# Performance work log

Hardware: AMD Instinct MI355X
Metric: run time of the kernel (lower is better)

The kernel has to match this reference:

```python
import jax, jax.numpy as jnp
import numpy as np

B, S, D, H = 2, 2048, 1024, 16
HD = D // H  # head dim = 64


def setup_inputs() -> dict:
    key = jax.random.key(0)
    ks = jax.random.split(key, 8)
    s = 0.02
    return {
        "Q": jax.random.normal(ks[0], (B, S, D), jnp.float32),
        "K": jax.random.normal(ks[1], (B, S, D), jnp.float32),
        "V": jax.random.normal(ks[2], (B, S, D), jnp.float32),
        "mask": jax.random.randint(ks[3], (1, 1, S, S), 0, 2, jnp.int32),
        "Wq": jax.random.normal(ks[4], (D, D), jnp.float32) * s,
        "bq": jnp.zeros((D,), jnp.float32),
        "Wk": jax.random.normal(ks[5], (D, D), jnp.float32) * s,
        "bk": jnp.zeros((D,), jnp.float32),
        "Wv": jax.random.normal(ks[6], (D, D), jnp.float32) * s,
        "bv": jnp.zeros((D,), jnp.float32),
        "Wo": jax.random.normal(ks[7], (D, D), jnp.float32) * s,
        "bo": jnp.zeros((D,), jnp.float32),
    }


def reference(Q, K, V, mask, Wq, bq, Wk, bk, Wv, bv, Wo, bo):
    b = Q.shape[0]
    # QKV projections, split into heads: [B,S,D] -> [B,H,S,HD]
    q = (Q @ Wq + bq).reshape(b, -1, H, HD).transpose(0, 2, 1, 3)
    k = (K @ Wk + bk).reshape(b, -1, H, HD).transpose(0, 2, 1, 3)
    v = (V @ Wv + bv).reshape(b, -1, H, HD).transpose(0, 2, 1, 3)
    # scaled dot-product attention with full [B,H,S,S] scores (as in source)
    scale = jnp.sqrt(jnp.asarray(HD, q.dtype))
    scores = jnp.einsum("bhqd,bhkd->bhqk", q, k) / scale
    scores = jnp.where(mask == 0, -jnp.inf, scores)
    attn = jax.nn.softmax(scores, axis=-1)
    ctx = jnp.einsum("bhqk,bhkd->bhqd", attn, v)
    # merge heads and output projection
    concat = ctx.transpose(0, 2, 1, 3).reshape(b, -1, H * HD)
    return concat @ Wo + bo
```

## Files before the change

### kernel.cpp

```cpp
#include <hip/hip_runtime.h>


using s8v = __attribute__((ext_vector_type(8))) short;
using f4v = __attribute__((ext_vector_type(4))) float;
typedef unsigned long long u64;

__device__ __forceinline__ unsigned short f2bf(float f) {
  union { float f; unsigned int u; } v; v.f = f;
  return (unsigned short)((v.u + 0x7fffu + ((v.u >> 16) & 1u)) >> 16);
}

__global__ void f2b3_kernel(const float* __restrict__ A, const float* __restrict__ B,
                            const float* __restrict__ C, unsigned short* __restrict__ oA,
                            unsigned short* __restrict__ oB, unsigned short* __restrict__ oC) {
  int z = blockIdx.x >> 12;
  int idx = (blockIdx.x & 4095) * 256 + threadIdx.x;
  const float* in = (z == 0) ? A : (z == 1) ? B : C;
  unsigned short* out = (z == 0) ? oA : (z == 1) ? oB : oC;
  float4 v = ((const float4*)in)[idx];
  ushort4 o;
  o.x = f2bf(v.x); o.y = f2bf(v.y); o.z = f2bf(v.z); o.w = f2bf(v.w);
  ((ushort4*)out)[idx] = o;
}

__global__ void packmask_kernel(const int* __restrict__ mask, u64* __restrict__ bm) {
  int gw = (int)((blockIdx.x * 256 + threadIdx.x) >> 6);
  int lane = threadIdx.x & 63;
  int mv = mask[(size_t)gw * 64 + lane];
  u64 bal = __ballot(mv != 0);
  if (lane == 0) bm[gw] = bal;
}

__global__ void wtrans4_kernel(const float* __restrict__ W0, const float* __restrict__ W1,
                               const float* __restrict__ W2, const float* __restrict__ W3,
                               unsigned short* __restrict__ T0, unsigned short* __restrict__ T1,
                               unsigned short* __restrict__ T2, unsigned short* __restrict__ T3) {
  __shared__ unsigned short t[64][72];
  int z = blockIdx.z;
  const float* W = (z == 0) ? W0 : (z == 1) ? W1 : (z == 2) ? W2 : W3;
  unsigned short* Wt = (z == 0) ? T0 : (z == 1) ? T1 : (z == 2) ? T2 : T3;
  int k0 = blockIdx.x * 64, n0 = blockIdx.y * 64;
  int tid = threadIdx.x;
  for (int p = 0; p < 4; ++p) {
    int idx = p * 256 + tid;
    int row = idx >> 4;
    int c4  = idx & 15;
    float4 v = *(const float4*)&W[(size_t)(k0 + row) * 1024 + n0 + c4 * 4];
    t[row][c4 * 4 + 0] = f2bf(v.x);
    t[row][c4 * 4 + 1] = f2bf(v.y);
    t[row][c4 * 4 + 2] = f2bf(v.z);
    t[row][c4 * 4 + 3] = f2bf(v.w);
  }
  __syncthreads();
  for (int p = 0; p < 2; ++p) {
    int idx = p * 256 + tid;
    int j  = idx >> 3;
    int c8 = idx & 7;
    unsigned short tmp[8];
    for (int i = 0; i < 8; ++i) tmp[i] = t[c8 * 8 + i][j];
    uint4 o;
    o.x = tmp[0] | ((unsigned)tmp[1] << 16);
    o.y = tmp[2] | ((unsigned)tmp[3] << 16);
    o.z = tmp[4] | ((unsigned)tmp[5] << 16);
    o.w = tmp[6] | ((unsigned)tmp[7] << 16);
    *(uint4*)&Wt[(size_t)(n0 + j) * 1024 + k0 + c8 * 8] = o;
  }
}

__global__ __launch_bounds__(256) void proj3_kernel(
    const unsigned short* __restrict__ A0, const unsigned short* __restrict__ A1,
    const unsigned short* __restrict__ A2,
    const unsigned short* __restrict__ W0, const unsigned short* __restrict__ W1,
    const unsigned short* __restrict__ W2,
    const float* __restrict__ b0, const float* __restrict__ b1, const float* __restrict__ b2,
    unsigned short* __restrict__ oq, unsigned short* __restrict__ ok,
    unsigned short* __restrict__ ovt) {
  const int z = blockIdx.z;
  const unsigned short* A  = (z == 0) ? A0 : (z == 1) ? A1 : A2;
  const unsigned short* Wt = (z == 0) ? W0 : (z == 1) ? W1 : W2;
  const float* bias        = (z == 0) ? b0 : (z == 1) ? b1 : b2;

  __shared__ __align__(16) unsigned short As[128][40];
  __shared__ __align__(16) unsigned short Bs[128][40];

  const int tid = threadIdx.x;
  const int lane = tid & 63, w = tid >> 6, ln = lane & 15, quad = lane >> 4;
  const int wm = (w & 1) * 64, wn = (w >> 1) * 64;
  const int m0 = blockIdx.x * 128, n0 = blockIdx.y * 128;

  const int r0 = tid >> 2, c40 = tid & 3;
  const int r1 = (tid + 256) >> 2, c41 = tid & 3;

  uint4 ar0 = *(const uint4*)&A[(size_t)(m0 + r0) * 1024 + c40 * 8];
  uint4 ar1 = *(const uint4*)&A[(size_t)(m0 + r1) * 1024 + c41 * 8];
  uint4 br0 = *(const uint4*)&Wt[(size_t)(n0 + r0) * 1024 + c40 * 8];
  uint4 br1 = *(const uint4*)&Wt[(size_t)(n0 + r1) * 1024 + c41 * 8];

  f4v zero = {0.f, 0.f, 0.f, 0.f};
  f4v acc[4][4];
  for (int mi = 0; mi < 4; ++mi)
    for (int ni = 0; ni < 4; ++ni) acc[mi][ni] = zero;

  for (int kt = 0; kt < 1024; kt += 32) {
    *(uint4*)&As[r0][c40 * 8] = ar0;
    *(uint4*)&As[r1][c41 * 8] = ar1;
    *(uint4*)&Bs[r0][c40 * 8] = br0;
    *(uint4*)&Bs[r1][c41 * 8] = br1;
    if (kt + 32 < 1024) {
      ar0 = *(const uint4*)&A[(size_t)(m0 + r0) * 1024 + kt + 32 + c40 * 8];
      ar1 = *(const uint4*)&A[(size_t)(m0 + r1) * 1024 + kt + 32 + c41 * 8];
      br0 = *(const uint4*)&Wt[(size_t)(n0 + r0) * 1024 + kt + 32 + c40 * 8];
      br1 = *(const uint4*)&Wt[(size_t)(n0 + r1) * 1024 + kt + 32 + c41 * 8];
    }
    __syncthreads();
    s8v a[4], b[4];
    for (int mi = 0; mi < 4; ++mi) a[mi] = *(const s8v*)&As[wm + mi * 16 + ln][quad * 8];
    for (int ni = 0; ni < 4; ++ni) b[ni] = *(const s8v*)&Bs[wn + ni * 16 + ln][quad * 8];
    for (int mi = 0; mi < 4; ++mi)
      for (int ni = 0; ni < 4; ++ni)
        acc[mi][ni] = __builtin_amdgcn_mfma_f32_16x16x32_bf16(a[mi], b[ni], acc[mi][ni], 0, 0, 0);
    __syncthreads();
  }

  const float qscale = (z == 0) ? 0.18033688f : 1.0f;
  if (z < 2) {
    unsigned short* outp = (z == 0) ? oq : ok;
    for (int mi = 0; mi < 4; ++mi) {
      int rb = m0 + wm + mi * 16 + quad * 4;
      int b_ = rb >> 11;
      for (int ni = 0; ni < 4; ++ni) {
        int col = n0 + wn + ni * 16 + ln;
        float bvv = bias[col];
        int h = col >> 6, hd = col & 63;
        size_t ob = (size_t)(b_ * 16 + h) * 2048;
        for (int r = 0; r < 4; ++r) {
          int s = (rb + r) & 2047;
          outp[(ob + s) * 64 + hd] = f2bf((acc[mi][ni][r] + bvv) * qscale);
        }
      }
    }
  } else {
    for (int mi = 0; mi < 4; ++mi) {
      int rb = m0 + wm + mi * 16 + quad * 4;
      int b_ = rb >> 11, s = rb & 2047;
      for (int ni = 0; ni < 4; ++ni) {
        int col = n0 + wn + ni * 16 + ln;
        float bvv = bias[col];
        int h = col >> 6, hd = col & 63;
        ushort4 o;
        o.x = f2bf(acc[mi][ni][0] + bvv);
        o.y = f2bf(acc[mi][ni][1] + bvv);
        o.z = f2bf(acc[mi][ni][2] + bvv);
        o.w = f2bf(acc[mi][ni][3] + bvv);
        *(ushort4*)&ovt[((size_t)(b_ * 16 + h) * 64 + hd) * 2048 + s] = o;
      }
    }
  }
}

__global__ __launch_bounds__(256) void flash_kernel(
    const unsigned short* __restrict__ q, const unsigned short* __restrict__ k,
    const unsigned short* __restrict__ vt, const u64* __restrict__ bm,
    unsigned short* __restrict__ ctx) {
  __shared__ __align__(16) unsigned short qp_s[128][72];
  __shared__ __align__(16) unsigned short k_s[64][72];
  __shared__ __align__(16) unsigned short v_s[64][72];

  const int tid = threadIdx.x;
  const int lane = tid & 63, w = tid >> 6, ln = lane & 15, quad = lane >> 4;
  const int q0 = blockIdx.x * 128;
  const int bh = blockIdx.y;
  const unsigned short* qg  = q  + ((size_t)bh * 2048 + q0) * 64;
  const unsigned short* kgb = k  + (size_t)bh * 2048 * 64;
  const unsigned short* vgb = vt + (size_t)bh * 64 * 2048;

  for (int p = 0; p < 4; ++p) {
    int c = p * 256 + tid;
    int row = c >> 3, c8 = c & 7;
    *(uint4*)&qp_s[row][c8 * 8] = *(const uint4*)&qg[(size_t)row * 64 + c8 * 8];
  }
  __syncthreads();
  s8v aq[2][2];
  for (int s = 0; s < 2; ++s)
    for (int h = 0; h < 2; ++h)
      aq[s][h] = *(const s8v*)&qp_s[s * 64 + w * 16 + ln][h * 32 + quad * 8];

  const int srow0 = tid >> 3, sc8 = tid & 7;
  const int srow1 = 32 + srow0;

  const u64* bmr0 = bm + (size_t)(q0 + w * 16 + ln) * 32;
  const u64* bmr1 = bmr0 + 64 * 32;

  uint4 kr0 = *(const uint4*)&kgb[(size_t)srow0 * 64 + sc8 * 8];
  uint4 kr1 = *(const uint4*)&kgb[(size_t)srow1 * 64 + sc8 * 8];
  uint4 vr0 = *(const uint4*)&vgb[(size_t)srow0 * 2048 + sc8 * 8];
  uint4 vr1 = *(const uint4*)&vgb[(size_t)srow1 * 2048 + sc8 * 8];
  u64 mwc[2], mwn[2];
  mwc[0] = bmr0[0];
  mwc[1] = bmr1[0];

  f4v zero = {0.f, 0.f, 0.f, 0.f};
  float lsum[2] = {0.f, 0.f};
  f4v o_acc[2][4];
  for (int s = 0; s < 2; ++s)
    for (int ni = 0; ni < 4; ++ni) o_acc[s][ni] = zero;

  for (int kt = 0; kt < 2048; kt += 64) {
    *(uint4*)&k_s[srow0][sc8 * 8] = kr0;
    *(uint4*)&k_s[srow1][sc8 * 8] = kr1;
    *(uint4*)&v_s[srow0][sc8 * 8] = vr0;
    *(uint4*)&v_s[srow1][sc8 * 8] = vr1;
    if (kt + 64 < 2048) {
      int ktn = kt + 64;
      kr0 = *(const uint4*)&kgb[(size_t)(ktn + srow0) * 64 + sc8 * 8];
      kr1 = *(const uint4*)&kgb[(size_t)(ktn + srow1) * 64 + sc8 * 8];
      vr0 = *(const uint4*)&vgb[(size_t)srow0 * 2048 + ktn + sc8 * 8];
      vr1 = *(const uint4*)&vgb[(size_t)srow1 * 2048 + ktn + sc8 * 8];
      int ktcn = ktn >> 6;
      mwn[0] = bmr0[ktcn];
      mwn[1] = bmr1[ktcn];
    }
    __syncthreads();

    f4v sc[2][4];
    for (int ni = 0; ni < 4; ++ni) {
      s8v ak0 = *(const s8v*)&k_s[ni * 16 + ln][quad * 8];
      s8v ak1 = *(const s8v*)&k_s[ni * 16 + ln][32 + quad * 8];
      for (int s = 0; s < 2; ++s) {
        f4v t = zero;
        t = __builtin_amdgcn_mfma_f32_16x16x32_bf16(ak0, aq[s][0], t, 0, 0, 0);
        t = __builtin_amdgcn_mfma_f32_16x16x32_bf16(ak1, aq[s][1], t, 0, 0, 0);
        sc[s][ni] = t;
      }
    }

    for (int s = 0; s < 2; ++s) {
      u64 m = mwc[s] >> (quad * 4);
      unsigned mlo = (unsigned)m, mhi = (unsigned)(m >> 32);
      float lacc = 0.f;
      for (int ni = 0; ni < 4; ++ni) {
        unsigned msel = ((ni < 2) ? mlo : mhi) >> ((ni & 1) * 16);
        u64 pk = 0;
        for (int r = 0; r < 4; ++r) {
          float e = __builtin_amdgcn_exp2f(sc[s][ni][r]) * (float)((msel >> r) & 1u);
          unsigned u = __float_as_uint(e);
          lacc += __uint_as_float(u & 0xffff0000u);
          pk |= (u64)(u >> 16) << (16 * r);
        }
        *(u64*)&qp_s[s * 64 + w * 16 + ln][ni * 16 + quad * 4] = pk;
      }
      lsum[s] += lacc;
      mwc[s] = mwn[s];
    }

    s8v ap[2][2];
    for (int s = 0; s < 2; ++s)
      for (int h = 0; h < 2; ++h)
        ap[s][h] = *(const s8v*)&qp_s[s * 64 + w * 16 + ln][h * 32 + quad * 8];
    for (int ni = 0; ni < 4; ++ni) {
      s8v bv0 = *(const s8v*)&v_s[ni * 16 + ln][quad * 8];
      s8v bv1 = *(const s8v*)&v_s[ni * 16 + ln][32 + quad * 8];
      for (int s = 0; s < 2; ++s) {
        o_acc[s][ni] = __builtin_amdgcn_mfma_f32_16x16x32_bf16(ap[s][0], bv0, o_acc[s][ni], 0, 0, 0);
        o_acc[s][ni] = __builtin_amdgcn_mfma_f32_16x16x32_bf16(ap[s][1], bv1, o_acc[s][ni], 0, 0, 0);
      }
    }
    __syncthreads();
  }

  int b_ = bh >> 4, h = bh & 15;
  for (int s = 0; s < 2; ++s) {
    float l = lsum[s];
    l += __shfl_xor(l, 16);
    l += __shfl_xor(l, 32);
    for (int r = 0; r < 4; ++r) {
      float lr = __shfl(l, quad * 4 + r);
      float inv = 1.f / lr;
      int srow = q0 + s * 64 + w * 16 + quad * 4 + r;
      size_t base = ((size_t)b_ * 2048 + srow) * 1024 + h * 64;
      for (int ni = 0; ni < 4; ++ni)
        ctx[base + ni * 16 + ln] = f2bf(o_acc[s][ni][r] * inv);
    }
  }
}

__global__ __launch_bounds__(256) void gemm_out_kernel(
    const unsigned short* __restrict__ A, const unsigned short* __restrict__ Wt,
    const float* __restrict__ bias, float* __restrict__ out) {
  __shared__ __align__(16) unsigned short As[128][40];
  __shared__ __align__(16) unsigned short Bs[128][40];

  const int tid = threadIdx.x;
  const int lane = tid & 63, w = tid >> 6, ln = lane & 15, quad = lane >> 4;
  const int wm = (w & 1) * 64, wn = (w >> 1) * 64;
  const int m0 = blockIdx.x * 128, n0 = blockIdx.y * 128;

  const int r0 = tid >> 2, c40 = tid & 3;
  const int r1 = (tid + 256) >> 2, c41 = tid & 3;

  uint4 ar0 = *(const uint4*)&A[(size_t)(m0 + r0) * 1024 + c40 * 8];
  uint4 ar1 = *(const uint4*)&A[(size_t)(m0 + r1) * 1024 + c41 * 8];
  uint4 br0 = *(const uint4*)&Wt[(size_t)(n0 + r0) * 1024 + c40 * 8];
  uint4 br1 = *(const uint4*)&Wt[(size_t)(n0 + r1) * 1024 + c41 * 8];

  f4v zero = {0.f, 0.f, 0.f, 0.f};
  f4v acc[4][4];
  for (int mi = 0; mi < 4; ++mi)
    for (int ni = 0; ni < 4; ++ni) acc[mi][ni] = zero;

  for (int kt = 0; kt < 1024; kt += 32) {
    *(uint4*)&As[r0][c40 * 8] = ar0;
    *(uint4*)&As[r1][c41 * 8] = ar1;
    *(uint4*)&Bs[r0][c40 * 8] = br0;
    *(uint4*)&Bs[r1][c41 * 8] = br1;
    if (kt + 32 < 1024) {
      ar0 = *(const uint4*)&A[(size_t)(m0 + r0) * 1024 + kt + 32 + c40 * 8];
      ar1 = *(const uint4*)&A[(size_t)(m0 + r1) * 1024 + kt + 32 + c41 * 8];
      br0 = *(const uint4*)&Wt[(size_t)(n0 + r0) * 1024 + kt + 32 + c40 * 8];
      br1 = *(const uint4*)&Wt[(size_t)(n0 + r1) * 1024 + kt + 32 + c41 * 8];
    }
    __syncthreads();
    s8v a[4], b[4];
    for (int mi = 0; mi < 4; ++mi) a[mi] = *(const s8v*)&As[wm + mi * 16 + ln][quad * 8];
    for (int ni = 0; ni < 4; ++ni) b[ni] = *(const s8v*)&Bs[wn + ni * 16 + ln][quad * 8];
    for (int mi = 0; mi < 4; ++mi)
      for (int ni = 0; ni < 4; ++ni)
        acc[mi][ni] = __builtin_amdgcn_mfma_f32_16x16x32_bf16(a[mi], b[ni], acc[mi][ni], 0, 0, 0);
    __syncthreads();
  }

  for (int mi = 0; mi < 4; ++mi) {
    int rb = m0 + wm + mi * 16 + quad * 4;
    for (int ni = 0; ni < 4; ++ni) {
      int col = n0 + wn + ni * 16 + ln;
      float bvv = bias[col];
      for (int r = 0; r < 4; ++r)
        out[(size_t)(rb + r) * 1024 + col] = acc[mi][ni][r] + bvv;
    }
  }
}

extern "C" void kernel_launch(void* const* d_in, const int* in_sizes, int n_in,
                              void* d_out, int out_size, void* d_ws, size_t ws_size,
                              hipStream_t stream) {
  const float* Q  = (const float*)d_in[0];
  const float* K  = (const float*)d_in[1];
  const float* V  = (const float*)d_in[2];
  const int* mask = (const int*)d_in[3];
  const float* Wq = (const float*)d_in[4];
  const float* bq = (const float*)d_in[5];
  const float* Wk = (const float*)d_in[6];
  const float* bk = (const float*)d_in[7];
  const float* Wv = (const float*)d_in[8];
  const float* bv = (const float*)d_in[9];
  const float* Wo = (const float*)d_in[10];
  const float* bo = (const float*)d_in[11];
  float* out = (float*)d_out;

  char* ws = (char*)d_ws;
  const size_t MB = 1u << 20;
  unsigned short* qb  = (unsigned short*)(ws + 0 * MB);
  unsigned short* kb  = (unsigned short*)(ws + 8 * MB);
  unsigned short* vb  = (unsigned short*)(ws + 16 * MB);
  unsigned short* wqt = (unsigned short*)(ws + 24 * MB);
  unsigned short* wkt = (unsigned short*)(ws + 26 * MB);
  unsigned short* wvt = (unsigned short*)(ws + 28 * MB);
  unsigned short* wot = (unsigned short*)(ws + 30 * MB);
  unsigned short* qh  = (unsigned short*)(ws + 32 * MB);
  unsigned short* kh  = (unsigned short*)(ws + 40 * MB);
  unsigned short* vth = (unsigned short*)(ws + 48 * MB);
  unsigned short* ctx = (unsigned short*)(ws + 56 * MB);
  u64* bm = (u64*)(ws + 0 * MB);

  f2b3_kernel<<<12288, 256, 0, stream>>>(Q, K, V, qb, kb, vb);
  wtrans4_kernel<<<dim3(16, 16, 4), 256, 0, stream>>>(Wq, Wk, Wv, Wo, wqt, wkt, wvt, wot);
  proj3_kernel<<<dim3(32, 8, 3), 256, 0, stream>>>(qb, kb, vb, wqt, wkt, wvt,
                                                   bq, bk, bv, qh, kh, vth);
  packmask_kernel<<<16384, 256, 0, stream>>>(mask, bm);
  flash_kernel<<<dim3(16, 32), 256, 0, stream>>>(qh, kh, vth, bm, ctx);
  gemm_out_kernel<<<dim3(32, 8), 256, 0, stream>>>(ctx, wot, bo, out);
}
```

Measured before the change: 270.8 us.

## Use direct global-to-LDS loads with swizzle, MFMA row sums, transposed V store

Both GEMM kernels now stage tiles with global_load_lds into an XOR-swizzled, unpadded LDS layout instead of register-staged loads, which drops the register prefetch and its software pipelining. The V projection swaps MFMA operands so the transposed V output is written with coalesced scalar stores along the sequence. The flash kernel computes softmax row sums with an extra MFMA against a ones matrix instead of scalar accumulation plus shuffles. It also packs exponentials to bf16 with perm instructions. This trades overlap of global loads with compute for lower VGPR use and fewer instructions, and adds MFMA work for the row sums.

```diff
diff --git a/kernel.cpp b/kernel.cpp
--- a/kernel.cpp
+++ b/kernel.cpp
@@ -8,6 +8,12 @@
 __device__ __forceinline__ unsigned short f2bf(float f) {
   union { float f; unsigned int u; } v; v.f = f;
   return (unsigned short)((v.u + 0x7fffu + ((v.u >> 16) & 1u)) >> 16);
+}
+
+__device__ __forceinline__ void gll16(const void* g, void* l) {
+  __builtin_amdgcn_global_load_lds(
+      (const __attribute__((address_space(1))) unsigned int*)g,
+      (__attribute__((address_space(3))) unsigned int*)l, 16, 0, 0);
 }
 
 __global__ void f2b3_kernel(const float* __restrict__ A, const float* __restrict__ B,
@@ -43,8 +49,7 @@
   int tid = threadIdx.x;
   for (int p = 0; p < 4; ++p) {
     int idx = p * 256 + tid;
-    int row = idx >> 4;
-    int c4  = idx & 15;
+    int row = idx >> 4, c4 = idx & 15;
     float4 v = *(const float4*)&W[(size_t)(k0 + row) * 1024 + n0 + c4 * 4];
     t[row][c4 * 4 + 0] = f2bf(v.x);
     t[row][c4 * 4 + 1] = f2bf(v.y);
@@ -54,8 +59,7 @@
   __syncthreads();
   for (int p = 0; p < 2; ++p) {
     int idx = p * 256 + tid;
-    int j  = idx >> 3;
-    int c8 = idx & 7;
+    int j = idx >> 3, c8 = idx & 7;
     unsigned short tmp[8];
     for (int i = 0; i < 8; ++i) tmp[i] = t[c8 * 8 + i][j];
     uint4 o;
@@ -80,21 +84,17 @@
   const unsigned short* Wt = (z == 0) ? W0 : (z == 1) ? W1 : W2;
   const float* bias        = (z == 0) ? b0 : (z == 1) ? b1 : b2;
 
-  __shared__ __align__(16) unsigned short As[128][40];
-  __shared__ __align__(16) unsigned short Bs[128][40];
+  __shared__ __align__(16) unsigned short As[128 * 32];
+  __shared__ __align__(16) unsigned short Bs[128 * 32];
 
   const int tid = threadIdx.x;
   const int lane = tid & 63, w = tid >> 6, ln = lane & 15, quad = lane >> 4;
   const int wm = (w & 1) * 64, wn = (w >> 1) * 64;
   const int m0 = blockIdx.x * 128, n0 = blockIdx.y * 128;
 
-  const int r0 = tid >> 2, c40 = tid & 3;
-  const int r1 = (tid + 256) >> 2, c41 = tid & 3;
-
-  uint4 ar0 = *(const uint4*)&A[(size_t)(m0 + r0) * 1024 + c40 * 8];
-  uint4 ar1 = *(const uint4*)&A[(size_t)(m0 + r1) * 1024 + c41 * 8];
-  uint4 br0 = *(const uint4*)&Wt[(size_t)(n0 + r0) * 1024 + c40 * 8];
-  uint4 br1 = *(const uint4*)&Wt[(size_t)(n0 + r1) * 1024 + c41 * 8];
+  const int srow = w * 32 + (lane >> 2);
+  const int schunk = (lane & 3) ^ ((lane >> 2) & 3);
+  const int cfrag = (quad ^ (ln & 3)) * 8;
 
   f4v zero = {0.f, 0.f, 0.f, 0.f};
   f4v acc[4][4];
@@ -102,28 +102,28 @@
     for (int ni = 0; ni < 4; ++ni) acc[mi][ni] = zero;
 
   for (int kt = 0; kt < 1024; kt += 32) {
-    *(uint4*)&As[r0][c40 * 8] = ar0;
-    *(uint4*)&As[r1][c41 * 8] = ar1;
-    *(uint4*)&Bs[r0][c40 * 8] = br0;
-    *(uint4*)&Bs[r1][c41 * 8] = br1;
-    if (kt + 32 < 1024) {
-      ar0 = *(const uint4*)&A[(size_t)(m0 + r0) * 1024 + kt + 32 + c40 * 8];
-      ar1 = *(const uint4*)&A[(size_t)(m0 + r1) * 1024 + kt + 32 + c41 * 8];
-      br0 = *(const uint4*)&Wt[(size_t)(n0 + r0) * 1024 + kt + 32 + c40 * 8];
-      br1 = *(const uint4*)&Wt[(size_t)(n0 + r1) * 1024 + kt + 32 + c41 * 8];
-    }
+    __syncthreads();
+    gll16(&A[(size_t)(m0 + srow) * 1024 + kt + schunk * 8],       &As[(w * 32) * 32]);
+    gll16(&A[(size_t)(m0 + srow + 16) * 1024 + kt + schunk * 8],  &As[(w * 32 + 16) * 32]);
+    gll16(&Wt[(size_t)(n0 + srow) * 1024 + kt + schunk * 8],      &Bs[(w * 32) * 32]);
+    gll16(&Wt[(size_t)(n0 + srow + 16) * 1024 + kt + schunk * 8], &Bs[(w * 32 + 16) * 32]);
     __syncthreads();
     s8v a[4], b[4];
-    for (int mi = 0; mi < 4; ++mi) a[mi] = *(const s8v*)&As[wm + mi * 16 + ln][quad * 8];
-    for (int ni = 0; ni < 4; ++ni) b[ni] = *(const s8v*)&Bs[wn + ni * 16 + ln][quad * 8];
-    for (int mi = 0; mi < 4; ++mi)
-      for (int ni = 0; ni < 4; ++ni)
-        acc[mi][ni] = __builtin_amdgcn_mfma_f32_16x16x32_bf16(a[mi], b[ni], acc[mi][ni], 0, 0, 0);
-    __syncthreads();
-  }
-
-  const float qscale = (z == 0) ? 0.18033688f : 1.0f;
+    for (int mi = 0; mi < 4; ++mi) a[mi] = *(const s8v*)&As[(wm + mi * 16 + ln) * 32 + cfrag];
+    for (int ni = 0; ni < 4; ++ni) b[ni] = *(const s8v*)&Bs[(wn + ni * 16 + ln) * 32 + cfrag];
+    if (z < 2) {
+      for (int mi = 0; mi < 4; ++mi)
+        for (int ni = 0; ni < 4; ++ni)
+          acc[mi][ni] = __builtin_amdgcn_mfma_f32_16x16x32_bf16(a[mi], b[ni], acc[mi][ni], 0, 0, 0);
+    } else {
+      for (int mi = 0; mi < 4; ++mi)
+        for (int ni = 0; ni < 4; ++ni)
+          acc[mi][ni] = __builtin_amdgcn_mfma_f32_16x16x32_bf16(b[ni], a[mi], acc[mi][ni], 0, 0, 0);
+    }
+  }
+
   if (z < 2) {
+    const float qscale = (z == 0) ? 0.18033688f : 1.0f;
     unsigned short* outp = (z == 0) ? oq : ok;
     for (int mi = 0; mi < 4; ++mi) {
       int rb = m0 + wm + mi * 16 + quad * 4;
@@ -140,19 +140,16 @@
       }
     }
   } else {
-    for (int mi = 0; mi < 4; ++mi) {
-      int rb = m0 + wm + mi * 16 + quad * 4;
-      int b_ = rb >> 11, s = rb & 2047;
-      for (int ni = 0; ni < 4; ++ni) {
-        int col = n0 + wn + ni * 16 + ln;
-        float bvv = bias[col];
-        int h = col >> 6, hd = col & 63;
-        ushort4 o;
-        o.x = f2bf(acc[mi][ni][0] + bvv);
-        o.y = f2bf(acc[mi][ni][1] + bvv);
-        o.z = f2bf(acc[mi][ni][2] + bvv);
-        o.w = f2bf(acc[mi][ni][3] + bvv);
-        *(ushort4*)&ovt[((size_t)(b_ * 16 + h) * 64 + hd) * 2048 + s] = o;
+    for (int ni = 0; ni < 4; ++ni) {
+      for (int r = 0; r < 4; ++r) {
+        int colw = n0 + wn + ni * 16 + quad * 4 + r;
+        int h = colw >> 6, hd = colw & 63;
+        float bvv = bias[colw];
+        for (int mi = 0; mi < 4; ++mi) {
+          int sg = m0 + wm + mi * 16 + ln;
+          int b_ = sg >> 11, ss = sg & 2047;
+          ovt[((size_t)(b_ * 16 + h) * 64 + hd) * 2048 + ss] = f2bf(acc[mi][ni][r] + bvv);
+        }
       }
     }
   }
@@ -164,7 +161,7 @@
     unsigned short* __restrict__ ctx) {
   __shared__ __align__(16) unsigned short qp_s[128][72];
   __shared__ __align__(16) unsigned short k_s[64][72];
-  __shared__ __align__(16) unsigned short v_s[64][72];
+  __shared__ __align__(16) unsigned short v_s[80][72];
 
   const int tid = threadIdx.x;
   const int lane = tid & 63, w = tid >> 6, ln = lane & 15, quad = lane >> 4;
@@ -174,16 +171,25 @@
   const unsigned short* kgb = k  + (size_t)bh * 2048 * 64;
   const unsigned short* vgb = vt + (size_t)bh * 64 * 2048;
 
+  for (int j = 0; j < 5; ++j) {
+    int idx = j * 256 + tid;
+    if (idx < 16 * 72) ((unsigned short*)v_s[64])[idx] = 0;
+  }
   for (int p = 0; p < 4; ++p) {
     int c = p * 256 + tid;
     int row = c >> 3, c8 = c & 7;
     *(uint4*)&qp_s[row][c8 * 8] = *(const uint4*)&qg[(size_t)row * 64 + c8 * 8];
   }
   __syncthreads();
+  if (tid < 64) v_s[64][tid] = 0x3F80;
+  __syncthreads();
+
   s8v aq[2][2];
   for (int s = 0; s < 2; ++s)
     for (int h = 0; h < 2; ++h)
       aq[s][h] = *(const s8v*)&qp_s[s * 64 + w * 16 + ln][h * 32 + quad * 8];
+  s8v bones0 = *(const s8v*)&v_s[64 + ln][quad * 8];
+  s8v bones1 = *(const s8v*)&v_s[64 + ln][32 + quad * 8];
 
   const int srow0 = tid >> 3, sc8 = tid & 7;
   const int srow1 = 32 + srow0;
@@ -200,10 +206,12 @@
   mwc[1] = bmr1[0];
 
   f4v zero = {0.f, 0.f, 0.f, 0.f};
-  float lsum[2] = {0.f, 0.f};
+  f4v l_acc[2];
   f4v o_acc[2][4];
-  for (int s = 0; s < 2; ++s)
+  for (int s = 0; s < 2; ++s) {
+    l_acc[s] = zero;
     for (int ni = 0; ni < 4; ++ni) o_acc[s][ni] = zero;
+  }
 
   for (int kt = 0; kt < 2048; kt += 64) {
     *(uint4*)&k_s[srow0][sc8 * 8] = kr0;
@@ -237,19 +245,16 @@
     for (int s = 0; s < 2; ++s) {
       u64 m = mwc[s] >> (quad * 4);
       unsigned mlo = (unsigned)m, mhi = (unsigned)(m >> 32);
-      float lacc = 0.f;
       for (int ni = 0; ni < 4; ++ni) {
         unsigned msel = ((ni < 2) ? mlo : mhi) >> ((ni & 1) * 16);
-        u64 pk = 0;
-        for (int r = 0; r < 4; ++r) {
-          float e = __builtin_amdgcn_exp2f(sc[s][ni][r]) * (float)((msel >> r) & 1u);
-          unsigned u = __float_as_uint(e);
-          lacc += __uint_as_float(u & 0xffff0000u);
-          pk |= (u64)(u >> 16) << (16 * r);
-        }
-        *(u64*)&qp_s[s * 64 + w * 16 + ln][ni * 16 + quad * 4] = pk;
-      }
-      lsum[s] += lacc;
+        unsigned u0 = __float_as_uint(__builtin_amdgcn_exp2f(sc[s][ni][0]) * (float)(msel & 1u));
+        unsigned u1 = __float_as_uint(__builtin_amdgcn_exp2f(sc[s][ni][1]) * (float)((msel >> 1) & 1u));
+        unsigned u2 = __float_as_uint(__builtin_amdgcn_exp2f(sc[s][ni][2]) * (float)((msel >> 2) & 1u));
+        unsigned u3 = __float_as_uint(__builtin_amdgcn_exp2f(sc[s][ni][3]) * (float)((msel >> 3) & 1u));
+        unsigned plo = __builtin_amdgcn_perm(u1, u0, 0x07060302);
+        unsigned phi = __builtin_amdgcn_perm(u3, u2, 0x07060302);
+        *(u64*)&qp_s[s * 64 + w * 16 + ln][ni * 16 + quad * 4] = plo | ((u64)phi << 32);
+      }
       mwc[s] = mwn[s];
     }
 
@@ -265,16 +270,17 @@
         o_acc[s][ni] = __builtin_amdgcn_mfma_f32_16x16x32_bf16(ap[s][1], bv1, o_acc[s][ni], 0, 0, 0);
       }
     }
+    for (int s = 0; s < 2; ++s) {
+      l_acc[s] = __builtin_amdgcn_mfma_f32_16x16x32_bf16(ap[s][0], bones0, l_acc[s], 0, 0, 0);
+      l_acc[s] = __builtin_amdgcn_mfma_f32_16x16x32_bf16(ap[s][1], bones1, l_acc[s], 0, 0, 0);
+    }
     __syncthreads();
   }
 
   int b_ = bh >> 4, h = bh & 15;
   for (int s = 0; s < 2; ++s) {
-    float l = lsum[s];
-    l += __shfl_xor(l, 16);
-    l += __shfl_xor(l, 32);
     for (int r = 0; r < 4; ++r) {
-      float lr = __shfl(l, quad * 4 + r);
+      float lr = __shfl(l_acc[s][r], quad * 16);
       float inv = 1.f / lr;
       int srow = q0 + s * 64 + w * 16 + quad * 4 + r;
       size_t base = ((size_t)b_ * 2048 + srow) * 1024 + h * 64;
@@ -287,21 +293,17 @@
 __global__ __launch_bounds__(256) void gemm_out_kernel(
     const unsigned short* __restrict__ A, const unsigned short* __restrict__ Wt,
     const float* __restrict__ bias, float* __restrict__ out) {
-  __shared__ __align__(16) unsigned short As[128][40];
-  __shared__ __align__(16) unsigned short Bs[128][40];
+  __shared__ __align__(16) unsigned short As[128 * 32];
+  __shared__ __align__(16) unsigned short Bs[128 * 32];
 
   const int tid = threadIdx.x;
   const int lane = tid & 63, w = tid >> 6, ln = lane & 15, quad = lane >> 4;
   const int wm = (w & 1) * 64, wn = (w >> 1) * 64;
   const int m0 = blockIdx.x * 128, n0 = blockIdx.y * 128;
 
-  const int r0 = tid >> 2, c40 = tid & 3;
-  const int r1 = (tid + 256) >> 2, c41 = tid & 3;
-
-  uint4 ar0 = *(const uint4*)&A[(size_t)(m0 + r0) * 1024 + c40 * 8];
-  uint4 ar1 = *(const uint4*)&A[(size_t)(m0 + r1) * 1024 + c41 * 8];
-  uint4 br0 = *(const uint4*)&Wt[(size_t)(n0 + r0) * 1024 + c40 * 8];
-  uint4 br1 = *(const uint4*)&Wt[(size_t)(n0 + r1) * 1024 + c41 * 8];
+  const int srow = w * 32 + (lane >> 2);
+  const int schunk = (lane & 3) ^ ((lane >> 2) & 3);
+  const int cfrag = (quad ^ (ln & 3)) * 8;
 
   f4v zero = {0.f, 0.f, 0.f, 0.f};
   f4v acc[4][4];
@@ -309,24 +311,18 @@
     for (int ni = 0; ni < 4; ++ni) acc[mi][ni] = zero;
 
   for (int kt = 0; kt < 1024; kt += 32) {
-    *(uint4*)&As[r0][c40 * 8] = ar0;
-    *(uint4*)&As[r1][c41 * 8] = ar1;
-    *(uint4*)&Bs[r0][c40 * 8] = br0;
-    *(uint4*)&Bs[r1][c41 * 8] = br1;
-    if (kt + 32 < 1024) {
-      ar0 = *(const uint4*)&A[(size_t)(m0 + r0) * 1024 + kt + 32 + c40 * 8];
-      ar1 = *(const uint4*)&A[(size_t)(m0 + r1) * 1024 + kt + 32 + c41 * 8];
-      br0 = *(const uint4*)&Wt[(size_t)(n0 + r0) * 1024 + kt + 32 + c40 * 8];
-      br1 = *(const uint4*)&Wt[(size_t)(n0 + r1) * 1024 + kt + 32 + c41 * 8];
-    }
+    __syncthreads();
+    gll16(&A[(size_t)(m0 + srow) * 1024 + kt + schunk * 8],       &As[(w * 32) * 32]);
+    gll16(&A[(size_t)(m0 + srow + 16) * 1024 + kt + schunk * 8],  &As[(w * 32 + 16) * 32]);
+    gll16(&Wt[(size_t)(n0 + srow) * 1024 + kt + schunk * 8],      &Bs[(w * 32) * 32]);
+    gll16(&Wt[(size_t)(n0 + srow + 16) * 1024 + kt + schunk * 8], &Bs[(w * 32 + 16) * 32]);
     __syncthreads();
     s8v a[4], b[4];
-    for (int mi = 0; mi < 4; ++mi) a[mi] = *(const s8v*)&As[wm + mi * 16 + ln][quad * 8];
-    for (int ni = 0; ni < 4; ++ni) b[ni] = *(const s8v*)&Bs[wn + ni * 16 + ln][quad * 8];
+    for (int mi = 0; mi < 4; ++mi) a[mi] = *(const s8v*)&As[(wm + mi * 16 + ln) * 32 + cfrag];
+    for (int ni = 0; ni < 4; ++ni) b[ni] = *(const s8v*)&Bs[(wn + ni * 16 + ln) * 32 + cfrag];
     for (int mi = 0; mi < 4; ++mi)
       for (int ni = 0; ni < 4; ++ni)
         acc[mi][ni] = __builtin_amdgcn_mfma_f32_16x16x32_bf16(a[mi], b[ni], acc[mi][ni], 0, 0, 0);
-    __syncthreads();
   }
 
   for (int mi = 0; mi < 4; ++mi) {
```

Measured after the change: 272.3 us. Within noise of the previous version (+0.6%).
